# Kernel tuning notes

Measured on AMD Instinct MI355X. Metric: run time of the kernel, lower is better.

## Reference

```python
import jax, jax.numpy as jnp
import numpy as np

EPS = 1e-6


def rms_norm(x, w):
    xf = x.astype(jnp.float32)
    var = jnp.mean(xf * xf, axis=-1, keepdims=True)
    return (xf * jax.lax.rsqrt(var + EPS)).astype(x.dtype) * w


def rope_interleaved(x, cos, sin):
    # x: [B, S, D]; rotate interleaved pairs (even=real, odd=imag)
    B, S, D = x.shape
    xp = x.reshape(B, S, D // 2, 2)
    rot = jnp.stack([-xp[..., 1], xp[..., 0]], axis=-1).reshape(B, S, D)
    return (x.astype(jnp.float32) * cos + rot.astype(jnp.float32) * sin).astype(x.dtype)


def setup_inputs() -> dict:
    key = jax.random.key(0)
    ks = jax.random.split(key, 8)
    B, S, D = 1, 2048, 2048
    H, Dh = 32, 64
    std = 1.0 / np.sqrt(D)

    hidden_states = jax.random.normal(ks[0], (B, S, D), jnp.float32)

    # interleaved RoPE tables tiled across heads -> [1, S, D]
    pos = np.arange(S, dtype=np.float64)
    inv_freq = 1.0 / (10000.0 ** (np.arange(0, Dh, 2, dtype=np.float64) / Dh))
    ang = pos[:, None] * inv_freq[None, :]          # [S, Dh/2]
    ang = np.repeat(ang, 2, axis=-1)                 # [S, Dh] interleaved
    ang = np.tile(ang, (1, H))                       # [S, D]
    cos = jnp.asarray(np.cos(ang)[None], jnp.float32)
    sin = jnp.asarray(np.sin(ang)[None], jnp.float32)

    Wq = jax.random.normal(ks[1], (D, D), jnp.float32) * std
    Wk = jax.random.normal(ks[2], (D, D), jnp.float32) * std
    Wv = jax.random.normal(ks[3], (D, D), jnp.float32) * std
    Wo = jax.random.normal(ks[4], (D, D), jnp.float32) * std
    bq = jax.random.normal(ks[5], (D,), jnp.float32) * 0.02
    bk = jax.random.normal(ks[6], (D,), jnp.float32) * 0.02
    bv = jax.random.normal(ks[7], (D,), jnp.float32) * 0.02
    bo = jnp.zeros((D,), jnp.float32)
    q_norm_w = jnp.ones((D,), jnp.float32)
    k_norm_w = jnp.ones((D,), jnp.float32)
    return {
        "hidden_states": hidden_states, "cos": cos, "sin": sin,
        "Wq": Wq, "bq": bq, "Wk": Wk, "bk": bk, "Wv": Wv, "bv": bv,
        "q_norm_w": q_norm_w, "k_norm_w": k_norm_w, "Wo": Wo, "bo": bo,
    }


def reference(hidden_states, cos, sin, Wq, bq, Wk, bk, Wv, bv, q_norm_w, k_norm_w, Wo, bo):
    B, S, D = hidden_states.shape
    H, Dh = 32, 64
    # QKV projections (self-attention: encoder_hidden_states = hidden_states)
    q = hidden_states @ Wq + bq
    k = hidden_states @ Wk + bk
    v = hidden_states @ Wv + bv
    # RMSNorm across heads (over full inner_dim)
    q = rms_norm(q, q_norm_w)
    k = rms_norm(k, k_norm_w)
    # interleaved rotary embedding (key uses query rope when key rope is None)
    q = rope_interleaved(q, cos, sin)
    k = rope_interleaved(k, cos, sin)
    # split heads: [B, H, S, Dh]
    q = q.reshape(B, S, H, Dh).transpose(0, 2, 1, 3)
    k = k.reshape(B, S, H, Dh).transpose(0, 2, 1, 3)
    v = v.reshape(B, S, H, Dh).transpose(0, 2, 1, 3)
    # scaled dot-product attention (no mask, not causal)
    scale = 1.0 / jnp.sqrt(jnp.asarray(Dh, q.dtype))
    scores = jnp.einsum("bhqd,bhkd->bhqk", q, k) * scale
    attn = jax.nn.softmax(scores, axis=-1)
    out = jnp.einsum("bhqk,bhkd->bhqd", attn, v)
    out = out.transpose(0, 2, 1, 3).reshape(B, S, H * Dh)
    return out @ Wo + bo
```

## Files before the change

### kernel.cpp

```cpp
#include <hip/hip_runtime.h>
#include <hip/hip_bf16.h>

typedef __bf16 bf16_t;
typedef __bf16 bf16x8 __attribute__((ext_vector_type(8)));
typedef __bf16 bf16x4 __attribute__((ext_vector_type(4)));
typedef float floatx4 __attribute__((ext_vector_type(4)));
typedef float floatx16 __attribute__((ext_vector_type(16)));

#define S_LEN 2048
#define D_DIM 2048
#define NHEADS 32
#define DH 64

__device__ __forceinline__ void gll16(const bf16_t* g, bf16_t* l) {
    __builtin_amdgcn_global_load_lds(
        (const __attribute__((address_space(1))) unsigned int*)g,
        (__attribute__((address_space(3))) unsigned int*)l, 16, 0, 0);
}

#define BAR()    asm volatile("s_barrier" ::: "memory")
#define WAIT(N)  asm volatile("s_waitcnt vmcnt(" #N ")" ::: "memory")
#define DSWAIT() asm volatile("s_waitcnt lgkmcnt(0)" ::: "memory")

__global__ __launch_bounds__(256) void k_cvt_bf16(const float* __restrict__ x,
                                                  bf16_t* __restrict__ y, int n) {
    int i = (blockIdx.x * 256 + threadIdx.x) * 8;
    if (i + 8 > n) return;
    const float4 a = *(const float4*)(x + i);
    const float4 b = *(const float4*)(x + i + 4);
    bf16x8 o;
    o[0] = (bf16_t)a.x; o[1] = (bf16_t)a.y; o[2] = (bf16_t)a.z; o[3] = (bf16_t)a.w;
    o[4] = (bf16_t)b.x; o[5] = (bf16_t)b.y; o[6] = (bf16_t)b.z; o[7] = (bf16_t)b.w;
    *(bf16x8*)(y + i) = o;
}

__global__ __launch_bounds__(256) void k_transpose4(
    const float* __restrict__ W0, const float* __restrict__ W1,
    const float* __restrict__ W2, const float* __restrict__ W3,
    bf16_t* __restrict__ T0, bf16_t* __restrict__ T1,
    bf16_t* __restrict__ T2, bf16_t* __restrict__ T3)
{
    const float* W; bf16_t* T;
    switch (blockIdx.z) {
        case 0: W = W0; T = T0; break;
        case 1: W = W1; T = T1; break;
        case 2: W = W2; T = T2; break;
        default: W = W3; T = T3; break;
    }
    __shared__ float tile[64][65];
    const int n0 = blockIdx.x * 64, k0 = blockIdx.y * 64;
    const int tx = threadIdx.x & 63, ty = threadIdx.x >> 6;
    #pragma unroll
    for (int i = 0; i < 16; ++i) {
        int r = i * 4 + ty;
        tile[r][tx] = W[(size_t)(k0 + r) * D_DIM + n0 + tx];
    }
    __syncthreads();
    #pragma unroll
    for (int i = 0; i < 16; ++i) {
        int r = i * 4 + ty;
        T[(size_t)(n0 + r) * D_DIM + k0 + tx] = (bf16_t)tile[tx][r];
    }
}

#define BM 128
#define BN 128
#define BK 32

__global__ __launch_bounds__(256) void k_gemm_qkv(
    const bf16_t* __restrict__ A,
    const bf16_t* __restrict__ Bt0, const bf16_t* __restrict__ Bt1, const bf16_t* __restrict__ Bt2,
    const float* __restrict__ bias0, const float* __restrict__ bias1, const float* __restrict__ bias2,
    bf16_t* __restrict__ Qout, bf16_t* __restrict__ Kout, bf16_t* __restrict__ VtOut,
    int M, int N, int K)
{
    const bf16_t* Bt; const float* bias;
    if (blockIdx.z == 0)      { Bt = Bt0; bias = bias0; }
    else if (blockIdx.z == 1) { Bt = Bt1; bias = bias1; }
    else                      { Bt = Bt2; bias = bias2; }

    __shared__ bf16_t As[3][BM][BK];
    __shared__ bf16_t Bs[3][BN][BK];

    const int t    = threadIdx.x;
    const int lane = t & 63;
    const int wave = t >> 6;
    const int wm = (wave >> 1) * 64;
    const int wn = (wave & 1) * 64;
    const int bm = blockIdx.y * BM;
    const int bn = blockIdx.x * BN;
    const int lm = lane & 15;
    const int lq = lane >> 4;

    const int srow0 = wave * 32 + (lane >> 2);
    const int srow1 = srow0 + 16;
    const int cp    = lane & 3;
    const int gc0 = cp ^ ((srow0 >> 1) & 3);
    const int gc1 = cp ^ ((srow1 >> 1) & 3);

    const bf16_t* Ag0 = A  + (size_t)(bm + srow0) * K + gc0 * 8;
    const bf16_t* Ag1 = A  + (size_t)(bm + srow1) * K + gc1 * 8;
    const bf16_t* Bg0 = Bt + (size_t)(bn + srow0) * K + gc0 * 8;
    const bf16_t* Bg1 = Bt + (size_t)(bn + srow1) * K + gc1 * 8;

    floatx4 acc[4][4];
    #pragma unroll
    for (int i = 0; i < 4; ++i)
        #pragma unroll
        for (int j = 0; j < 4; ++j)
            #pragma unroll
            for (int r = 0; r < 4; ++r) acc[i][j][r] = 0.f;

    const int NIT = K / BK;
    auto stage = [&](int buf, int k0) {
        gll16(Ag0 + k0, &As[buf][wave * 32][0]);
        gll16(Ag1 + k0, &As[buf][wave * 32 + 16][0]);
        gll16(Bg0 + k0, &Bs[buf][wave * 32][0]);
        gll16(Bg1 + k0, &Bs[buf][wave * 32 + 16][0]);
    };
    stage(0, 0);
    stage(1, BK);

    for (int i = 0; i < NIT; ++i) {
        BAR();
        if (i + 2 < NIT) {
            stage((i + 2) % 3, (i + 2) * BK);
            WAIT(8);
        } else if (i + 1 < NIT) {
            WAIT(4);
        } else {
            WAIT(0);
        }
        BAR();

        const int buf = i % 3;
        bf16x8 af[4], bfr[4];
        #pragma unroll
        for (int ii = 0; ii < 4; ++ii) {
            const int row = wm + ii * 16 + lm;
            af[ii] = *(const bf16x8*)&As[buf][row][(lq ^ ((row >> 1) & 3)) * 8];
        }
        #pragma unroll
        for (int j = 0; j < 4; ++j) {
            const int row = wn + j * 16 + lm;
            bfr[j] = *(const bf16x8*)&Bs[buf][row][(lq ^ ((row >> 1) & 3)) * 8];
        }
        #pragma unroll
        for (int ii = 0; ii < 4; ++ii)
            #pragma unroll
            for (int j = 0; j < 4; ++j)
                acc[ii][j] = __builtin_amdgcn_mfma_f32_16x16x32_bf16(af[ii], bfr[j], acc[ii][j], 0, 0, 0);
    }

    if (blockIdx.z == 2) {
        #pragma unroll
        for (int i = 0; i < 4; ++i) {
            const int row0 = bm + wm + i * 16 + lq * 4;
            #pragma unroll
            for (int j = 0; j < 4; ++j) {
                const int col = bn + wn + j * 16 + lm;
                const float bb = bias[col];
                bf16x4 pk;
                #pragma unroll
                for (int r = 0; r < 4; ++r) pk[r] = (bf16_t)(acc[i][j][r] + bb);
                *(bf16x4*)(VtOut + (size_t)col * M + row0) = pk;
            }
        }
    } else {
        bf16_t* C = (blockIdx.z == 0) ? Qout : Kout;
        #pragma unroll
        for (int i = 0; i < 4; ++i) {
            const int row0 = bm + wm + i * 16 + lq * 4;
            #pragma unroll
            for (int j = 0; j < 4; ++j) {
                const int col = bn + wn + j * 16 + lm;
                const float bb = bias[col];
                #pragma unroll
                for (int r = 0; r < 4; ++r)
                    C[(size_t)(row0 + r) * N + col] = (bf16_t)(acc[i][j][r] + bb);
            }
        }
    }
}

__global__ __launch_bounds__(256) void k_gemm_splitk(
    const bf16_t* __restrict__ A, const bf16_t* __restrict__ Bt,
    float* __restrict__ P0, float* __restrict__ P1, float* __restrict__ P2,
    int M, int N, int K)
{
    __shared__ bf16_t As[3][BM][BK];
    __shared__ bf16_t Bs[3][BN][BK];

    const int t    = threadIdx.x;
    const int lane = t & 63;
    const int wave = t >> 6;
    const int wm = (wave >> 1) * 64;
    const int wn = (wave & 1) * 64;
    const int bm = blockIdx.y * BM;
    const int bn = blockIdx.x * BN;
    const int lm = lane & 15;
    const int lq = lane >> 4;
    const int z  = blockIdx.z;

    const int nit_all = K / BK;
    const int it0 = (z * nit_all) / 3;
    const int it1 = ((z + 1) * nit_all) / 3;
    const int NIT = it1 - it0;
    const int kbase = it0 * BK;

    const int srow0 = wave * 32 + (lane >> 2);
    const int srow1 = srow0 + 16;
    const int cp    = lane & 3;
    const int gc0 = cp ^ ((srow0 >> 1) & 3);
    const int gc1 = cp ^ ((srow1 >> 1) & 3);

    const bf16_t* Ag0 = A  + (size_t)(bm + srow0) * K + kbase + gc0 * 8;
    const bf16_t* Ag1 = A  + (size_t)(bm + srow1) * K + kbase + gc1 * 8;
    const bf16_t* Bg0 = Bt + (size_t)(bn + srow0) * K + kbase + gc0 * 8;
    const bf16_t* Bg1 = Bt + (size_t)(bn + srow1) * K + kbase + gc1 * 8;

    floatx4 acc[4][4];
    #pragma unroll
    for (int i = 0; i < 4; ++i)
        #pragma unroll
        for (int j = 0; j < 4; ++j)
            #pragma unroll
            for (int r = 0; r < 4; ++r) acc[i][j][r] = 0.f;

    auto stage = [&](int buf, int k0) {
        gll16(Ag0 + k0, &As[buf][wave * 32][0]);
        gll16(Ag1 + k0, &As[buf][wave * 32 + 16][0]);
        gll16(Bg0 + k0, &Bs[buf][wave * 32][0]);
        gll16(Bg1 + k0, &Bs[buf][wave * 32 + 16][0]);
    };
    stage(0, 0);
    if (1 < NIT) stage(1, BK);

    for (int i = 0; i < NIT; ++i) {
        BAR();
        if (i + 2 < NIT) {
            stage((i + 2) % 3, (i + 2) * BK);
            WAIT(8);
        } else if (i + 1 < NIT) {
            WAIT(4);
        } else {
            WAIT(0);
        }
        BAR();

        const int buf = i % 3;
        bf16x8 af[4], bfr[4];
        #pragma unroll
        for (int ii = 0; ii < 4; ++ii) {
            const int row = wm + ii * 16 + lm;
            af[ii] = *(const bf16x8*)&As[buf][row][(lq ^ ((row >> 1) & 3)) * 8];
        }
        #pragma unroll
        for (int j = 0; j < 4; ++j) {
            const int row = wn + j * 16 + lm;
            bfr[j] = *(const bf16x8*)&Bs[buf][row][(lq ^ ((row >> 1) & 3)) * 8];
        }
        #pragma unroll
        for (int ii = 0; ii < 4; ++ii)
            #pragma unroll
            for (int j = 0; j < 4; ++j)
                acc[ii][j] = __builtin_amdgcn_mfma_f32_16x16x32_bf16(af[ii], bfr[j], acc[ii][j], 0, 0, 0);
    }

    float* C = (z == 0) ? P0 : (z == 1) ? P1 : P2;
    #pragma unroll
    for (int i = 0; i < 4; ++i) {
        const int row0 = bm + wm + i * 16 + lq * 4;
        #pragma unroll
        for (int j = 0; j < 4; ++j) {
            const int col = bn + wn + j * 16 + lm;
            #pragma unroll
            for (int r = 0; r < 4; ++r)
                C[(size_t)(row0 + r) * N + col] = acc[i][j][r];
        }
    }
}

__global__ __launch_bounds__(256) void k_reduce_bias(
    const float* __restrict__ P0, const float* __restrict__ P1,
    const float* __restrict__ P2, const float* __restrict__ bias,
    float* __restrict__ out)
{
    const int i = (blockIdx.x * 256 + threadIdx.x) * 4;
    const float4 b  = *(const float4*)(bias + (i & (D_DIM - 1)));
    const float4 a0 = *(const float4*)(P0 + i);
    const float4 a1 = *(const float4*)(P1 + i);
    const float4 a2 = *(const float4*)(P2 + i);
    float4 o;
    o.x = b.x + a0.x + a1.x + a2.x;
    o.y = b.y + a0.y + a1.y + a2.y;
    o.z = b.z + a0.z + a1.z + a2.z;
    o.w = b.w + a0.w + a1.w + a2.w;
    *(float4*)(out + i) = o;
}

__global__ __launch_bounds__(256) void k_norm_rope(
    bf16_t* __restrict__ Q, bf16_t* __restrict__ Kb_,
    const float* __restrict__ qw, const float* __restrict__ kw,
    const float* __restrict__ cosb, const float* __restrict__ sinb)
{
    bf16_t* X = (blockIdx.z == 0) ? Q : Kb_;
    const float* w = (blockIdx.z == 0) ? qw : kw;
    const int row = blockIdx.x;
    const int t = threadIdx.x;
    const size_t base = (size_t)row * D_DIM + t * 8;

    const bf16x8 xv = *(const bf16x8*)(X + base);
    float x[8];
    #pragma unroll
    for (int i = 0; i < 8; ++i) x[i] = (float)xv[i];

    float ss = 0.f;
    #pragma unroll
    for (int i = 0; i < 8; ++i) ss += x[i] * x[i];
    #pragma unroll
    for (int off = 32; off; off >>= 1) ss += __shfl_xor(ss, off);
    __shared__ float red[4];
    if ((t & 63) == 0) red[t >> 6] = ss;
    __syncthreads();
    const float tot = red[0] + red[1] + red[2] + red[3];
    const float rms = rsqrtf(tot * (1.0f / D_DIM) + 1e-6f);

    float wv[8], c[8], sn[8];
    { float4 a = *(const float4*)(w + t * 8); float4 b = *(const float4*)(w + t * 8 + 4);
      wv[0]=a.x; wv[1]=a.y; wv[2]=a.z; wv[3]=a.w; wv[4]=b.x; wv[5]=b.y; wv[6]=b.z; wv[7]=b.w; }
    const size_t cbase = (size_t)row * D_DIM + ((t * 8) & 63);
    { float4 a = *(const float4*)(cosb + cbase); float4 b = *(const float4*)(cosb + cbase + 4);
      c[0]=a.x; c[1]=a.y; c[2]=a.z; c[3]=a.w; c[4]=b.x; c[5]=b.y; c[6]=b.z; c[7]=b.w; }
    { float4 a = *(const float4*)(sinb + cbase); float4 b = *(const float4*)(sinb + cbase + 4);
      sn[0]=a.x; sn[1]=a.y; sn[2]=a.z; sn[3]=a.w; sn[4]=b.x; sn[5]=b.y; sn[6]=b.z; sn[7]=b.w; }

    bf16x8 o;
    #pragma unroll
    for (int p = 0; p < 4; ++p) {
        const float e  = x[2*p]     * rms * wv[2*p];
        const float od = x[2*p + 1] * rms * wv[2*p + 1];
        o[2*p]     = (bf16_t)(e * c[2*p]     - od * sn[2*p]);
        o[2*p + 1] = (bf16_t)(od * c[2*p + 1] + e * sn[2*p + 1]);
    }
    *(bf16x8*)(X + base) = o;
}

#define LDPQ 72

__global__ __launch_bounds__(256) void k_flash(
    const bf16_t* __restrict__ Qb, const bf16_t* __restrict__ Kb,
    const bf16_t* __restrict__ Vt, bf16_t* __restrict__ Ob)
{
    const int bid = blockIdx.x;
    const int jj  = bid >> 3;
    const int h   = ((bid & 7) << 2) | (jj >> 4);
    const int qblk = jj & 15;
    const int hc = h * DH;
    const int t = threadIdx.x;
    const int wave = t >> 6, lane = t & 63;
    const int ln = lane & 31, hf = lane >> 5;
    const int qw = qblk * 128 + wave * 32;

    __shared__ bf16_t Ks[3][64][64];
    __shared__ bf16_t Vs[3][64][64];
    __shared__ bf16_t Ps[4][32][LDPQ];
    __shared__ float  Lw[4][32];

    bf16x8 bq[4];
    #pragma unroll
    for (int kt = 0; kt < 4; ++kt)
        bq[kt] = *(const bf16x8*)(Qb + (size_t)(qw + ln) * D_DIM + hc + kt * 16 + hf * 8);

    const int r0  = wave * 16 + (lane >> 3);
    const int r1  = r0 + 8;
    const int cp8 = lane & 7;
    const int gcA = cp8 ^ (r0 & 7);
    const int gcB = cp8 ^ (r1 & 7);
    const bf16_t* kg0 = Kb + (size_t)r0 * D_DIM + hc + gcA * 8;
    const bf16_t* kg1 = Kb + (size_t)r1 * D_DIM + hc + gcB * 8;
    const bf16_t* vg0 = Vt + (size_t)(hc + r0) * S_LEN + gcA * 8;
    const bf16_t* vg1 = Vt + (size_t)(hc + r1) * S_LEN + gcB * 8;

    auto stageKV = [&](int buf, int kc) {
        gll16(kg0 + (size_t)kc * D_DIM, &Ks[buf][wave * 16][0]);
        gll16(kg1 + (size_t)kc * D_DIM, &Ks[buf][wave * 16 + 8][0]);
        gll16(vg0 + kc, &Vs[buf][wave * 16][0]);
        gll16(vg1 + kc, &Vs[buf][wave * 16 + 8][0]);
    };

    floatx16 o0, o1;
    #pragma unroll
    for (int r = 0; r < 16; ++r) { o0[r] = 0.f; o1[r] = 0.f; }
    float lsum = 0.f;

    const int swz = ln & 7;
    const float c_exp = 0.125f * 1.44269504089f;

    stageKV(0, 0);
    stageKV(1, 64);

    for (int kc = 0; kc < S_LEN; kc += 64) {
        const int cur = (kc >> 6) % 3;
        BAR();
        if (kc + 128 < S_LEN) {
            stageKV((kc / 64 + 2) % 3, kc + 128);
            WAIT(8);
        } else if (kc + 64 < S_LEN) {
            WAIT(4);
        } else {
            WAIT(0);
        }
        BAR();

        floatx16 st0, st1;
        #pragma unroll
        for (int r = 0; r < 16; ++r) { st0[r] = 0.f; st1[r] = 0.f; }
        #pragma unroll
        for (int kt = 0; kt < 4; ++kt) {
            const int ch = 2 * kt + hf;
            const bf16x8 a0 = *(const bf16x8*)&Ks[cur][ln]     [(ch ^ swz) * 8];
            const bf16x8 a1 = *(const bf16x8*)&Ks[cur][32 + ln][(ch ^ swz) * 8];
            st0 = __builtin_amdgcn_mfma_f32_32x32x16_bf16(a0, bq[kt], st0, 0, 0, 0);
            st1 = __builtin_amdgcn_mfma_f32_32x32x16_bf16(a1, bq[kt], st1, 0, 0, 0);
        }

        #pragma unroll
        for (int g = 0; g < 4; ++g) {
            bf16x4 p0, p1;
            #pragma unroll
            for (int r4 = 0; r4 < 4; ++r4) {
                const float e0 = __builtin_amdgcn_exp2f(st0[4 * g + r4] * c_exp);
                const float e1 = __builtin_amdgcn_exp2f(st1[4 * g + r4] * c_exp);
                p0[r4] = (bf16_t)e0; p1[r4] = (bf16_t)e1;
                lsum += e0 + e1;
            }
            *(bf16x4*)&Ps[wave][ln][8 * g + 4 * hf]      = p0;
            *(bf16x4*)&Ps[wave][ln][32 + 8 * g + 4 * hf] = p1;
        }
        DSWAIT();

        #pragma unroll
        for (int kt = 0; kt < 4; ++kt) {
            const int ch = 2 * kt + hf;
            const bf16x8 ap  = *(const bf16x8*)&Ps[wave][ln][kt * 16 + hf * 8];
            const bf16x8 bv0 = *(const bf16x8*)&Vs[cur][ln]     [(ch ^ swz) * 8];
            const bf16x8 bv1 = *(const bf16x8*)&Vs[cur][32 + ln][(ch ^ swz) * 8];
            o0 = __builtin_amdgcn_mfma_f32_32x32x16_bf16(ap, bv0, o0, 0, 0, 0);
            o1 = __builtin_amdgcn_mfma_f32_32x32x16_bf16(ap, bv1, o1, 0, 0, 0);
        }
    }

    const float ltot = lsum + __shfl_xor(lsum, 32);
    if (hf == 0) Lw[wave][ln] = ltot;
    DSWAIT();
    float4 li[4];
    li[0] = *(const float4*)&Lw[wave][4 * hf];
    li[1] = *(const float4*)&Lw[wave][8 + 4 * hf];
    li[2] = *(const float4*)&Lw[wave][16 + 4 * hf];
    li[3] = *(const float4*)&Lw[wave][24 + 4 * hf];

    #pragma unroll
    for (int r = 0; r < 16; ++r) {
        const int row = (r & 3) + 8 * (r >> 2) + 4 * hf;
        const float lv = (r & 3) == 0 ? li[r >> 2].x : (r & 3) == 1 ? li[r >> 2].y
                       : (r & 3) == 2 ? li[r >> 2].z : li[r >> 2].w;
        const float inv = 1.0f / lv;
        Ob[(size_t)(qw + row) * D_DIM + hc + ln]      = (bf16_t)(o0[r] * inv);
        Ob[(size_t)(qw + row) * D_DIM + hc + 32 + ln] = (bf16_t)(o1[r] * inv);
    }
}

extern "C" void kernel_launch(void* const* d_in, const int* in_sizes, int n_in,
                              void* d_out, int out_size, void* d_ws, size_t ws_size,
                              hipStream_t stream) {
    const float* hs   = (const float*)d_in[0];
    const float* cosb = (const float*)d_in[1];
    const float* sinb = (const float*)d_in[2];
    const float* Wq   = (const float*)d_in[3];
    const float* bq   = (const float*)d_in[4];
    const float* Wk   = (const float*)d_in[5];
    const float* bk   = (const float*)d_in[6];
    const float* Wv   = (const float*)d_in[7];
    const float* bv   = (const float*)d_in[8];
    const float* qw   = (const float*)d_in[9];
    const float* kw   = (const float*)d_in[10];
    const float* Wo   = (const float*)d_in[11];
    const float* bo   = (const float*)d_in[12];
    float* out = (float*)d_out;

    char* ws = (char*)d_ws;
    bf16_t* Xb  = (bf16_t*)(ws);
    bf16_t* Wqt = (bf16_t*)(ws + ((size_t)8  << 20));
    bf16_t* Wkt = (bf16_t*)(ws + ((size_t)16 << 20));
    bf16_t* Wvt = (bf16_t*)(ws + ((size_t)24 << 20));
    bf16_t* Wot = (bf16_t*)(ws + ((size_t)32 << 20));
    bf16_t* Qb  = (bf16_t*)(ws + ((size_t)40 << 20));
    bf16_t* Kb  = (bf16_t*)(ws + ((size_t)48 << 20));
    bf16_t* Vt  = (bf16_t*)(ws + ((size_t)56 << 20));
    bf16_t* Ob  = (bf16_t*)(ws + ((size_t)64 << 20));
    float*  P0  = (float*) (ws);
    float*  P1  = (float*) (ws + ((size_t)16 << 20));
    float*  P2  = (float*) (ws + ((size_t)48 << 20));

    const int n = S_LEN * D_DIM;

    k_cvt_bf16<<<n / (256 * 8), 256, 0, stream>>>(hs, Xb, n);
    k_transpose4<<<dim3(32, 32, 4), 256, 0, stream>>>(Wq, Wk, Wv, Wo, Wqt, Wkt, Wvt, Wot);

    k_gemm_qkv<<<dim3(D_DIM / BN, S_LEN / BM, 3), 256, 0, stream>>>(
        Xb, Wqt, Wkt, Wvt, bq, bk, bv, Qb, Kb, Vt, S_LEN, D_DIM, D_DIM);

    k_norm_rope<<<dim3(S_LEN, 1, 2), 256, 0, stream>>>(Qb, Kb, qw, kw, cosb, sinb);

    k_flash<<<512, 256, 0, stream>>>(Qb, Kb, Vt, Ob);

    k_gemm_splitk<<<dim3(D_DIM / BN, S_LEN / BM, 3), 256, 0, stream>>>(
        Ob, Wot, P0, P1, P2, S_LEN, D_DIM, D_DIM);
    k_reduce_bias<<<n / (256 * 4), 256, 0, stream>>>(P0, P1, P2, bo, out);
}
```

Measured before the change: 321.5 us.

## Software-pipeline flash attention QK with softmax/PV and fuse prep kernels

Restructures the flash attention loop so the QK^T MFMAs for the next key chunk are issued before the exponentiation and PV product of the previous chunk, using ping-pong score registers. The aim is to hide exp/LDS latency behind matrix work. Prefetch distance shrinks to one chunk ahead, and live register pressure rises. The bf16 conversion of the input and the weight transposes are merged into one launch, and the transpose now writes vectorised bf16x4 stores from a padded transposed tile.

```diff
diff --git a/kernel.cpp b/kernel.cpp
--- a/kernel.cpp
+++ b/kernel.cpp
@@ -22,24 +22,30 @@
 #define WAIT(N)  asm volatile("s_waitcnt vmcnt(" #N ")" ::: "memory")
 #define DSWAIT() asm volatile("s_waitcnt lgkmcnt(0)" ::: "memory")
 
-__global__ __launch_bounds__(256) void k_cvt_bf16(const float* __restrict__ x,
-                                                  bf16_t* __restrict__ y, int n) {
-    int i = (blockIdx.x * 256 + threadIdx.x) * 8;
-    if (i + 8 > n) return;
-    const float4 a = *(const float4*)(x + i);
-    const float4 b = *(const float4*)(x + i + 4);
-    bf16x8 o;
-    o[0] = (bf16_t)a.x; o[1] = (bf16_t)a.y; o[2] = (bf16_t)a.z; o[3] = (bf16_t)a.w;
-    o[4] = (bf16_t)b.x; o[5] = (bf16_t)b.y; o[6] = (bf16_t)b.z; o[7] = (bf16_t)b.w;
-    *(bf16x8*)(y + i) = o;
-}
-
-__global__ __launch_bounds__(256) void k_transpose4(
+__global__ __launch_bounds__(256) void k_prep(
+    const float* __restrict__ hs, bf16_t* __restrict__ Xb,
     const float* __restrict__ W0, const float* __restrict__ W1,
     const float* __restrict__ W2, const float* __restrict__ W3,
     bf16_t* __restrict__ T0, bf16_t* __restrict__ T1,
     bf16_t* __restrict__ T2, bf16_t* __restrict__ T3)
 {
+    const int t = threadIdx.x;
+    if (blockIdx.z == 4) {
+        const int bid = blockIdx.y * 32 + blockIdx.x;
+        const int i = (bid * 256 + t) * 16;
+        const float4 a0 = *(const float4*)(hs + i);
+        const float4 a1 = *(const float4*)(hs + i + 4);
+        const float4 a2 = *(const float4*)(hs + i + 8);
+        const float4 a3 = *(const float4*)(hs + i + 12);
+        bf16x8 o0, o1;
+        o0[0]=(bf16_t)a0.x; o0[1]=(bf16_t)a0.y; o0[2]=(bf16_t)a0.z; o0[3]=(bf16_t)a0.w;
+        o0[4]=(bf16_t)a1.x; o0[5]=(bf16_t)a1.y; o0[6]=(bf16_t)a1.z; o0[7]=(bf16_t)a1.w;
+        o1[0]=(bf16_t)a2.x; o1[1]=(bf16_t)a2.y; o1[2]=(bf16_t)a2.z; o1[3]=(bf16_t)a2.w;
+        o1[4]=(bf16_t)a3.x; o1[5]=(bf16_t)a3.y; o1[6]=(bf16_t)a3.z; o1[7]=(bf16_t)a3.w;
+        *(bf16x8*)(Xb + i) = o0;
+        *(bf16x8*)(Xb + i + 8) = o1;
+        return;
+    }
     const float* W; bf16_t* T;
     switch (blockIdx.z) {
         case 0: W = W0; T = T0; break;
@@ -47,19 +53,23 @@
         case 2: W = W2; T = T2; break;
         default: W = W3; T = T3; break;
     }
-    __shared__ float tile[64][65];
+    __shared__ float tile_t[64][68];
     const int n0 = blockIdx.x * 64, k0 = blockIdx.y * 64;
-    const int tx = threadIdx.x & 63, ty = threadIdx.x >> 6;
     #pragma unroll
     for (int i = 0; i < 16; ++i) {
-        int r = i * 4 + ty;
-        tile[r][tx] = W[(size_t)(k0 + r) * D_DIM + n0 + tx];
+        const int r = i * 4 + (t >> 6);
+        const int c = t & 63;
+        tile_t[c][r] = W[(size_t)(k0 + r) * D_DIM + n0 + c];
     }
     __syncthreads();
     #pragma unroll
-    for (int i = 0; i < 16; ++i) {
-        int r = i * 4 + ty;
-        T[(size_t)(n0 + r) * D_DIM + k0 + tx] = (bf16_t)tile[tx][r];
+    for (int j = 0; j < 4; ++j) {
+        const int n  = j * 16 + (t >> 4);
+        const int k4 = (t & 15) * 4;
+        const float4 v = *(const float4*)&tile_t[n][k4];
+        bf16x4 pk;
+        pk[0] = (bf16_t)v.x; pk[1] = (bf16_t)v.y; pk[2] = (bf16_t)v.z; pk[3] = (bf16_t)v.w;
+        *(bf16x4*)(T + (size_t)(n0 + n) * D_DIM + k0 + k4) = pk;
     }
 }
 
@@ -396,60 +406,79 @@
 
     const int swz = ln & 7;
     const float c_exp = 0.125f * 1.44269504089f;
-
-    stageKV(0, 0);
-    stageKV(1, 64);
-
-    for (int kc = 0; kc < S_LEN; kc += 64) {
-        const int cur = (kc >> 6) % 3;
-        BAR();
-        if (kc + 128 < S_LEN) {
-            stageKV((kc / 64 + 2) % 3, kc + 128);
-            WAIT(8);
-        } else if (kc + 64 < S_LEN) {
-            WAIT(4);
-        } else {
-            WAIT(0);
-        }
-        BAR();
-
-        floatx16 st0, st1;
-        #pragma unroll
-        for (int r = 0; r < 16; ++r) { st0[r] = 0.f; st1[r] = 0.f; }
+    const int NCH = S_LEN / 64;
+
+    auto qk = [&](int buf, floatx16& s0, floatx16& s1) {
+        #pragma unroll
+        for (int r = 0; r < 16; ++r) { s0[r] = 0.f; s1[r] = 0.f; }
         #pragma unroll
         for (int kt = 0; kt < 4; ++kt) {
             const int ch = 2 * kt + hf;
-            const bf16x8 a0 = *(const bf16x8*)&Ks[cur][ln]     [(ch ^ swz) * 8];
-            const bf16x8 a1 = *(const bf16x8*)&Ks[cur][32 + ln][(ch ^ swz) * 8];
-            st0 = __builtin_amdgcn_mfma_f32_32x32x16_bf16(a0, bq[kt], st0, 0, 0, 0);
-            st1 = __builtin_amdgcn_mfma_f32_32x32x16_bf16(a1, bq[kt], st1, 0, 0, 0);
-        }
-
+            const bf16x8 a0 = *(const bf16x8*)&Ks[buf][ln]     [(ch ^ swz) * 8];
+            const bf16x8 a1 = *(const bf16x8*)&Ks[buf][32 + ln][(ch ^ swz) * 8];
+            s0 = __builtin_amdgcn_mfma_f32_32x32x16_bf16(a0, bq[kt], s0, 0, 0, 0);
+            s1 = __builtin_amdgcn_mfma_f32_32x32x16_bf16(a1, bq[kt], s1, 0, 0, 0);
+        }
+    };
+    auto expv = [&](const floatx16& s0, const floatx16& s1) {
         #pragma unroll
         for (int g = 0; g < 4; ++g) {
             bf16x4 p0, p1;
             #pragma unroll
             for (int r4 = 0; r4 < 4; ++r4) {
-                const float e0 = __builtin_amdgcn_exp2f(st0[4 * g + r4] * c_exp);
-                const float e1 = __builtin_amdgcn_exp2f(st1[4 * g + r4] * c_exp);
+                const float e0 = __builtin_amdgcn_exp2f(s0[4 * g + r4] * c_exp);
+                const float e1 = __builtin_amdgcn_exp2f(s1[4 * g + r4] * c_exp);
                 p0[r4] = (bf16_t)e0; p1[r4] = (bf16_t)e1;
                 lsum += e0 + e1;
             }
             *(bf16x4*)&Ps[wave][ln][8 * g + 4 * hf]      = p0;
             *(bf16x4*)&Ps[wave][ln][32 + 8 * g + 4 * hf] = p1;
         }
-        DSWAIT();
-
+    };
+    auto pv = [&](int buf) {
         #pragma unroll
         for (int kt = 0; kt < 4; ++kt) {
             const int ch = 2 * kt + hf;
             const bf16x8 ap  = *(const bf16x8*)&Ps[wave][ln][kt * 16 + hf * 8];
-            const bf16x8 bv0 = *(const bf16x8*)&Vs[cur][ln]     [(ch ^ swz) * 8];
-            const bf16x8 bv1 = *(const bf16x8*)&Vs[cur][32 + ln][(ch ^ swz) * 8];
+            const bf16x8 bv0 = *(const bf16x8*)&Vs[buf][ln]     [(ch ^ swz) * 8];
+            const bf16x8 bv1 = *(const bf16x8*)&Vs[buf][32 + ln][(ch ^ swz) * 8];
             o0 = __builtin_amdgcn_mfma_f32_32x32x16_bf16(ap, bv0, o0, 0, 0, 0);
             o1 = __builtin_amdgcn_mfma_f32_32x32x16_bf16(ap, bv1, o1, 0, 0, 0);
         }
-    }
+    };
+
+    stageKV(0, 0);
+    stageKV(1, 64);
+
+    floatx16 stA0, stA1, stB0, stB1;
+
+    auto pipe_step = [&](int c, floatx16& n0_, floatx16& n1_,
+                         floatx16& p0_, floatx16& p1_) {
+        BAR();
+        if (c >= 1 && c + 1 < NCH) {
+            stageKV((c + 1) % 3, (c + 1) * 64);
+            WAIT(4);
+        } else if (c == 0) {
+            WAIT(4);
+        } else {
+            WAIT(0);
+        }
+        BAR();
+        qk(c % 3, n0_, n1_);
+        if (c > 0) {
+            expv(p0_, p1_);
+            DSWAIT();
+            pv((c - 1) % 3);
+        }
+    };
+
+    for (int c2 = 0; c2 < NCH; c2 += 2) {
+        pipe_step(c2,     stA0, stA1, stB0, stB1);
+        pipe_step(c2 + 1, stB0, stB1, stA0, stA1);
+    }
+    expv(stB0, stB1);
+    DSWAIT();
+    pv((NCH - 1) % 3);
 
     const float ltot = lsum + __shfl_xor(lsum, 32);
     if (hf == 0) Lw[wave][ln] = ltot;
@@ -505,8 +534,7 @@
 
     const int n = S_LEN * D_DIM;
 
-    k_cvt_bf16<<<n / (256 * 8), 256, 0, stream>>>(hs, Xb, n);
-    k_transpose4<<<dim3(32, 32, 4), 256, 0, stream>>>(Wq, Wk, Wv, Wo, Wqt, Wkt, Wvt, Wot);
+    k_prep<<<dim3(32, 32, 5), 256, 0, stream>>>(hs, Xb, Wq, Wk, Wv, Wo, Wqt, Wkt, Wvt, Wot);
 
     k_gemm_qkv<<<dim3(D_DIM / BN, S_LEN / BM, 3), 256, 0, stream>>>(
         Xb, Wqt, Wkt, Wvt, bq, bk, bv, Qb, Kb, Vt, S_LEN, D_DIM, D_DIM);
```

After: 314.0 us. -2.3%, faster.
